# Performance work log

Measured on AMD Instinct MI355X. Metric: run time of the kernel, lower is better.

The kernel has to match this reference:

```python
import jax, jax.numpy as jnp
import numpy as np

N_MID, EMB_DIM, HID, SEQ_LEN, BATCH = 200000, 128, 128, 256, 512


def setup_inputs() -> dict:
    key = jax.random.key(0)
    k1, k2, k3, k4, k5, k6, k7 = jax.random.split(key, 7)
    mid = jax.random.randint(k1, (BATCH,), 0, N_MID, dtype=jnp.int32)
    mid_hist = jax.random.randint(k2, (BATCH, SEQ_LEN), 0, N_MID, dtype=jnp.int32)
    mask = jax.random.randint(k3, (BATCH, SEQ_LEN), 0, 2, dtype=jnp.int32)
    # Embedding table: RandomUniform(-0.05, 0.05) per original init
    emb_table = jax.random.uniform(k4, (N_MID, EMB_DIM), jnp.float32, -0.05, 0.05)
    # Keras GRU (reset_after=True): kernel [D,3H], recurrent_kernel [H,3H], bias [2,3H]
    W = jax.random.normal(k5, (EMB_DIM, 3 * HID), jnp.float32) * 0.05
    U = jax.random.normal(k6, (HID, 3 * HID), jnp.float32) * 0.05
    b = jax.random.normal(k7, (2, 3 * HID), jnp.float32) * 0.05
    return {"mid": mid, "mid_hist": mid_hist, "mask": mask,
            "emb_table": emb_table, "W": W, "U": U, "b": b}


def _masked_gru(hist_emb, mask, W, U, b):
    # hist_emb: [B, T, D], mask: [B, T] int
    B, T, _ = hist_emb.shape
    H = U.shape[0]
    b_in, b_rec = b[0], b[1]
    # precompute input projections once: [B, T, 3H]
    x_proj = jnp.einsum('btd,dh->bth', hist_emb, W) + b_in
    x_proj_t = jnp.swapaxes(x_proj, 0, 1)  # [T, B, 3H]
    mask_t = jnp.swapaxes(mask, 0, 1).astype(bool)  # [T, B]

    def step(h, inp):
        x_t, m_t = inp
        rec = h @ U + b_rec  # [B, 3H]
        xz, xr, xh = x_t[:, :H], x_t[:, H:2 * H], x_t[:, 2 * H:]
        rz, rr, rh = rec[:, :H], rec[:, H:2 * H], rec[:, 2 * H:]
        z = jax.nn.sigmoid(xz + rz)
        r = jax.nn.sigmoid(xr + rr)
        hh = jnp.tanh(xh + r * rh)  # reset_after=True: r applied after recurrent matmul
        h_new = z * h + (1.0 - z) * hh
        h = jnp.where(m_t[:, None], h_new, h)  # masked steps hold state
        return h, None

    h0 = jnp.zeros((B, H), hist_emb.dtype)
    h_final, _ = jax.lax.scan(step, h0, (x_proj_t, mask_t))
    return h_final


def reference(mid, mid_hist, mask, emb_table, W, U, b):
    item_emb = emb_table[mid]            # [B, D]
    hist_emb = emb_table[mid_hist]       # [B, T, D]
    user_vec = _masked_gru(hist_emb, mask, W, U, b)  # [B, H]
    return (user_vec, item_emb)
```

## Files before the change

### kernel.cpp

```cpp
#include <hip/hip_runtime.h>

#define BATCH  512
#define SEQLEN 256
#define EMB    128
#define HID    128

typedef _Float16 f16;
typedef __attribute__((ext_vector_type(8))) _Float16 half8;
typedef __attribute__((ext_vector_type(4))) _Float16 half4f;
typedef __attribute__((ext_vector_type(4))) float    floatx4;

#define L2E 1.44269504088896340736f
#define T2E 2.88539008177792681472f

__device__ __forceinline__ int swzB(int byte) {
    return byte ^ (((byte >> 8) & 7) << 4);
}

__global__ void prep_kernel(const int* __restrict__ mask, const int* __restrict__ mid,
                            const float* __restrict__ emb,
                            unsigned* __restrict__ maskP, float* __restrict__ item_out) {
    const int bid = blockIdx.x, tid = threadIdx.x;
    if (bid < 32) {
        __shared__ int mls[16 * 256];
        for (int i = tid; i < 16 * 256; i += 256)
            mls[i] = mask[bid * 16 * 256 + i];
        __syncthreads();
        int t = tid;
        unsigned m = 0;
        #pragma unroll
        for (int r = 0; r < 16; ++r)
            m |= (unsigned)(mls[r * 256 + t] & 1) << r;
        maskP[bid * 256 + t] = m;
    } else {
        for (int i = (bid - 32) * 256 + tid; i < BATCH * EMB; i += 224 * 256) {
            int b = i >> 7, d = i & 127;
            item_out[i] = emb[(size_t)mid[b] * EMB + d];
        }
    }
}

__global__ __launch_bounds__(512, 2) void gru_fused(
        const int* __restrict__ mid_hist, const float* __restrict__ emb,
        const float* __restrict__ W, const float* __restrict__ U,
        const float* __restrict__ bvec, const unsigned* __restrict__ maskP,
        float* __restrict__ out_user) {
    __shared__ __align__(16) f16 hpk[2][16 * 128];
    __shared__ __align__(16) f16 elds[4][16 * 128];

    const int tid   = threadIdx.x;
    const int lane  = tid & 63;
    const int w     = tid >> 6;
    const int l15   = lane & 15;
    const int g4    = lane >> 4;
    const int blk   = blockIdx.x;
    const int bbase = blk * 16;

    half8 uA[3][4], wA[3][4];
    #pragma unroll
    for (int p = 0; p < 3; ++p)
        #pragma unroll
        for (int kt = 0; kt < 4; ++kt) {
            half8 u, v;
            const int j = p * 128 + w * 16 + l15;
            #pragma unroll
            for (int e = 0; e < 8; ++e) {
                int k = kt * 32 + g4 * 8 + e;
                u[e] = (f16)U[k * 384 + j];
                v[e] = (f16)W[k * 384 + j];
            }
            uA[p][kt] = u; wA[p][kt] = v;
        }

    const int jj = w * 16 + g4 * 4;
    float nbz[4], nbr[4], sxh[4], srh[4];
    {
        float4 a0 = *(const float4*)(bvec + jj);
        float4 a1 = *(const float4*)(bvec + 384 + jj);
        float4 c0 = *(const float4*)(bvec + 128 + jj);
        float4 c1 = *(const float4*)(bvec + 512 + jj);
        float4 d0 = *(const float4*)(bvec + 256 + jj);
        float4 d1 = *(const float4*)(bvec + 640 + jj);
        nbz[0] = -L2E*(a0.x+a1.x); nbz[1] = -L2E*(a0.y+a1.y);
        nbz[2] = -L2E*(a0.z+a1.z); nbz[3] = -L2E*(a0.w+a1.w);
        nbr[0] = -L2E*(c0.x+c1.x); nbr[1] = -L2E*(c0.y+c1.y);
        nbr[2] = -L2E*(c0.z+c1.z); nbr[3] = -L2E*(c0.w+c1.w);
        sxh[0] =  T2E*d0.x; sxh[1] = T2E*d0.y; sxh[2] = T2E*d0.z; sxh[3] = T2E*d0.w;
        srh[0] =  T2E*d1.x; srh[1] = T2E*d1.y; srh[2] = T2E*d1.z; srh[3] = T2E*d1.w;
    }

    int aswz[4];
    #pragma unroll
    for (int kt = 0; kt < 4; ++kt)
        aswz[kt] = swzB(l15 * 256 + kt * 64 + g4 * 16) >> 1;
    const int hswz = swzB(l15 * 256 + jj * 2) >> 1;
    const int r_e  = tid >> 5;
    const int c32  = tid & 31;
    const int sswz = swzB(r_e * 256 + c32 * 8) >> 1;
    const int histbase = (bbase + r_e) * SEQLEN;
    const int mpbase   = blk * SEQLEN;

    for (int i = tid; i < 16 * 128; i += 512) hpk[0][i] = (f16)0.f;

    {
        int i0 = mid_hist[histbase + 0];
        int i1 = mid_hist[histbase + 1];
        float4 v0 = *(const float4*)(emb + (size_t)i0 * EMB + c32 * 4);
        float4 v1 = *(const float4*)(emb + (size_t)i1 * EMB + c32 * 4);
        *(half4f*)&elds[0][sswz] = half4f{(f16)v0.x,(f16)v0.y,(f16)v0.z,(f16)v0.w};
        *(half4f*)&elds[1][sswz] = half4f{(f16)v1.x,(f16)v1.y,(f16)v1.z,(f16)v1.w};
    }
    int i2 = mid_hist[histbase + 2];
    int i3 = mid_hist[histbase + 3];
    float4   Ee = *(const float4*)(emb + (size_t)i2 * EMB + c32 * 4);
    float4   Eo = *(const float4*)(emb + (size_t)i3 * EMB + c32 * 4);
    int      Ie = mid_hist[histbase + 4];
    int      Io = mid_hist[histbase + 5];
    unsigned Me = maskP[mpbase + 0];
    unsigned Mo = maskP[mpbase + 1];

    float hreg[4] = {0.f, 0.f, 0.f, 0.f};
    __syncthreads();

    half8 ea[4];
    #pragma unroll
    for (int kt = 0; kt < 4; ++kt) ea[kt] = *(const half8*)&elds[0][aswz[kt]];

    auto step = [&](int t, float4& E, int& I, unsigned& M) {
        const f16* hrd = hpk[t & 1];
        f16*       hwr = hpk[(t + 1) & 1];
        half8 ha[4];
        #pragma unroll
        for (int kt = 0; kt < 4; ++kt) ha[kt] = *(const half8*)&hrd[aswz[kt]];

        floatx4 az = {0,0,0,0}, ar = {0,0,0,0}, axh = {0,0,0,0}, arh = {0,0,0,0};
        #pragma unroll
        for (int kt = 0; kt < 4; ++kt) {
            az  = __builtin_amdgcn_mfma_f32_16x16x32_f16(wA[0][kt], ea[kt], az,  0,0,0);
            ar  = __builtin_amdgcn_mfma_f32_16x16x32_f16(wA[1][kt], ea[kt], ar,  0,0,0);
            axh = __builtin_amdgcn_mfma_f32_16x16x32_f16(wA[2][kt], ea[kt], axh, 0,0,0);
        }
        #pragma unroll
        for (int kt = 0; kt < 4; ++kt) {
            az  = __builtin_amdgcn_mfma_f32_16x16x32_f16(uA[0][kt], ha[kt], az,  0,0,0);
            ar  = __builtin_amdgcn_mfma_f32_16x16x32_f16(uA[1][kt], ha[kt], ar,  0,0,0);
            arh = __builtin_amdgcn_mfma_f32_16x16x32_f16(uA[2][kt], ha[kt], arh, 0,0,0);
        }

        *(half4f*)&elds[(t + 2) & 3][sswz] =
            half4f{(f16)E.x, (f16)E.y, (f16)E.z, (f16)E.w};
        int ii = I;
        E = *(const float4*)(emb + (size_t)ii * EMB + c32 * 4);
        int t6 = t + 6 < SEQLEN ? t + 6 : SEQLEN - 1;
        I = mid_hist[histbase + t6];
        unsigned mval = M;
        M = maskP[mpbase + t + 2];
        {
            const f16* erd = elds[(t + 1) & 3];
            #pragma unroll
            for (int kt = 0; kt < 4; ++kt) ea[kt] = *(const half8*)&erd[aswz[kt]];
        }

        const int mbit = (mval >> l15) & 1;
        #pragma unroll
        for (int r = 0; r < 4; ++r) {
            float z  = __builtin_amdgcn_rcpf(1.f + __builtin_amdgcn_exp2f(__builtin_fmaf(az[r], -L2E, nbz[r])));
            float rg = __builtin_amdgcn_rcpf(1.f + __builtin_amdgcn_exp2f(__builtin_fmaf(ar[r], -L2E, nbr[r])));
            float u  = __builtin_fmaf(rg, __builtin_fmaf(arh[r], T2E, srh[r]),
                                          __builtin_fmaf(axh[r], T2E, sxh[r]));
            float hh = __builtin_fmaf(-2.f, __builtin_amdgcn_rcpf(__builtin_amdgcn_exp2f(u) + 1.f), 1.f);
            float hn = __builtin_fmaf(z, hreg[r] - hh, hh);
            hreg[r]  = mbit ? hn : hreg[r];
        }
        *(half4f*)&hwr[hswz] = half4f{(f16)hreg[0], (f16)hreg[1], (f16)hreg[2], (f16)hreg[3]};

        __builtin_amdgcn_sched_barrier(0);
        asm volatile("s_waitcnt lgkmcnt(0)" ::: "memory");
        __builtin_amdgcn_s_barrier();
        __builtin_amdgcn_sched_barrier(0);
    };

    #pragma unroll 1
    for (int t = 0; t < SEQLEN; t += 2) {
        step(t,     Ee, Ie, Me);
        step(t + 1, Eo, Io, Mo);
    }

    float4 o = { hreg[0], hreg[1], hreg[2], hreg[3] };
    *(float4*)(out_user + (size_t)(bbase + l15) * HID + jj) = o;
}

extern "C" void kernel_launch(void* const* d_in, const int* in_sizes, int n_in,
                              void* d_out, int out_size, void* d_ws, size_t ws_size,
                              hipStream_t stream) {
    const int*   mid      = (const int*)d_in[0];
    const int*   mid_hist = (const int*)d_in[1];
    const int*   mask     = (const int*)d_in[2];
    const float* emb      = (const float*)d_in[3];
    const float* W        = (const float*)d_in[4];
    const float* U        = (const float*)d_in[5];
    const float* bvec     = (const float*)d_in[6];

    float* user_out = (float*)d_out;
    float* item_out = (float*)d_out + BATCH * HID;

    unsigned* maskP = (unsigned*)d_ws;

    prep_kernel<<<256, 256, 0, stream>>>(mask, mid, emb, maskP, item_out);
    gru_fused  <<<32, 512, 0, stream>>>(mid_hist, emb, W, U, bvec, maskP, user_out);
}
```

Before: 353.1 us.

## Precompute next step's input projection MFMAs off the recurrent critical path

Moves the W·x input-projection MFMAs for step t+1 into step t, after the recurrent U·h MFMAs, so each step's dependent chain starts directly from h. The log2e/2log2e activation scales are folded into the fp16 W and U weights, which removes per-element scaling FMAs in the gate math. The cost is more live accumulator registers (two XAcc sets) and slightly different fp16 rounding of the weights. The mask prefetch index is also clamped to avoid reading past the end.

Result: no change. 355.8 us (+0.8%).

```diff
diff --git a/kernel.cpp b/kernel.cpp
--- a/kernel.cpp
+++ b/kernel.cpp
@@ -16,6 +16,8 @@
 __device__ __forceinline__ int swzB(int byte) {
     return byte ^ (((byte >> 8) & 7) << 4);
 }
+
+struct XAcc { floatx4 z, r, h; };
 
 __global__ void prep_kernel(const int* __restrict__ mask, const int* __restrict__ mid,
                             const float* __restrict__ emb,
@@ -58,7 +60,8 @@
 
     half8 uA[3][4], wA[3][4];
     #pragma unroll
-    for (int p = 0; p < 3; ++p)
+    for (int p = 0; p < 3; ++p) {
+        const float s = (p == 2) ? T2E : -L2E;
         #pragma unroll
         for (int kt = 0; kt < 4; ++kt) {
             half8 u, v;
@@ -66,11 +69,12 @@
             #pragma unroll
             for (int e = 0; e < 8; ++e) {
                 int k = kt * 32 + g4 * 8 + e;
-                u[e] = (f16)U[k * 384 + j];
-                v[e] = (f16)W[k * 384 + j];
+                u[e] = (f16)(U[k * 384 + j] * s);
+                v[e] = (f16)(W[k * 384 + j] * s);
             }
             uA[p][kt] = u; wA[p][kt] = v;
         }
+    }
 
     const int jj = w * 16 + g4 * 4;
     float nbz[4], nbr[4], sxh[4], srh[4];
@@ -122,29 +126,47 @@
     float hreg[4] = {0.f, 0.f, 0.f, 0.f};
     __syncthreads();
 
-    half8 ea[4];
-    #pragma unroll
-    for (int kt = 0; kt < 4; ++kt) ea[kt] = *(const half8*)&elds[0][aswz[kt]];
-
-    auto step = [&](int t, float4& E, int& I, unsigned& M) {
+    XAcc xA, xB;
+    {
+        half8 e0[4];
+        #pragma unroll
+        for (int kt = 0; kt < 4; ++kt) e0[kt] = *(const half8*)&elds[0][aswz[kt]];
+        xA.z = floatx4{0,0,0,0}; xA.r = floatx4{0,0,0,0}; xA.h = floatx4{0,0,0,0};
+        #pragma unroll
+        for (int kt = 0; kt < 4; ++kt) {
+            xA.z = __builtin_amdgcn_mfma_f32_16x16x32_f16(wA[0][kt], e0[kt], xA.z, 0,0,0);
+            xA.r = __builtin_amdgcn_mfma_f32_16x16x32_f16(wA[1][kt], e0[kt], xA.r, 0,0,0);
+            xA.h = __builtin_amdgcn_mfma_f32_16x16x32_f16(wA[2][kt], e0[kt], xA.h, 0,0,0);
+        }
+    }
+
+    auto step = [&](int t, XAcc& xc, XAcc& xn, float4& E, int& I, unsigned& M) {
         const f16* hrd = hpk[t & 1];
         f16*       hwr = hpk[(t + 1) & 1];
+
         half8 ha[4];
         #pragma unroll
         for (int kt = 0; kt < 4; ++kt) ha[kt] = *(const half8*)&hrd[aswz[kt]];
-
-        floatx4 az = {0,0,0,0}, ar = {0,0,0,0}, axh = {0,0,0,0}, arh = {0,0,0,0};
+        floatx4 arh = {0,0,0,0};
         #pragma unroll
         for (int kt = 0; kt < 4; ++kt) {
-            az  = __builtin_amdgcn_mfma_f32_16x16x32_f16(wA[0][kt], ea[kt], az,  0,0,0);
-            ar  = __builtin_amdgcn_mfma_f32_16x16x32_f16(wA[1][kt], ea[kt], ar,  0,0,0);
-            axh = __builtin_amdgcn_mfma_f32_16x16x32_f16(wA[2][kt], ea[kt], axh, 0,0,0);
-        }
-        #pragma unroll
-        for (int kt = 0; kt < 4; ++kt) {
-            az  = __builtin_amdgcn_mfma_f32_16x16x32_f16(uA[0][kt], ha[kt], az,  0,0,0);
-            ar  = __builtin_amdgcn_mfma_f32_16x16x32_f16(uA[1][kt], ha[kt], ar,  0,0,0);
-            arh = __builtin_amdgcn_mfma_f32_16x16x32_f16(uA[2][kt], ha[kt], arh, 0,0,0);
+            xc.z = __builtin_amdgcn_mfma_f32_16x16x32_f16(uA[0][kt], ha[kt], xc.z, 0,0,0);
+            xc.r = __builtin_amdgcn_mfma_f32_16x16x32_f16(uA[1][kt], ha[kt], xc.r, 0,0,0);
+            arh  = __builtin_amdgcn_mfma_f32_16x16x32_f16(uA[2][kt], ha[kt], arh,  0,0,0);
+        }
+
+        {
+            const f16* erd = elds[(t + 1) & 3];
+            half8 ea[4];
+            #pragma unroll
+            for (int kt = 0; kt < 4; ++kt) ea[kt] = *(const half8*)&erd[aswz[kt]];
+            xn.z = floatx4{0,0,0,0}; xn.r = floatx4{0,0,0,0}; xn.h = floatx4{0,0,0,0};
+            #pragma unroll
+            for (int kt = 0; kt < 4; ++kt) {
+                xn.z = __builtin_amdgcn_mfma_f32_16x16x32_f16(wA[0][kt], ea[kt], xn.z, 0,0,0);
+                xn.r = __builtin_amdgcn_mfma_f32_16x16x32_f16(wA[1][kt], ea[kt], xn.r, 0,0,0);
+                xn.h = __builtin_amdgcn_mfma_f32_16x16x32_f16(wA[2][kt], ea[kt], xn.h, 0,0,0);
+            }
         }
 
         *(half4f*)&elds[(t + 2) & 3][sswz] =
@@ -154,20 +176,15 @@
         int t6 = t + 6 < SEQLEN ? t + 6 : SEQLEN - 1;
         I = mid_hist[histbase + t6];
         unsigned mval = M;
-        M = maskP[mpbase + t + 2];
-        {
-            const f16* erd = elds[(t + 1) & 3];
-            #pragma unroll
-            for (int kt = 0; kt < 4; ++kt) ea[kt] = *(const half8*)&erd[aswz[kt]];
-        }
+        int tm = t + 2 < SEQLEN ? t + 2 : SEQLEN - 1;
+        M = maskP[mpbase + tm];
 
         const int mbit = (mval >> l15) & 1;
         #pragma unroll
         for (int r = 0; r < 4; ++r) {
-            float z  = __builtin_amdgcn_rcpf(1.f + __builtin_amdgcn_exp2f(__builtin_fmaf(az[r], -L2E, nbz[r])));
-            float rg = __builtin_amdgcn_rcpf(1.f + __builtin_amdgcn_exp2f(__builtin_fmaf(ar[r], -L2E, nbr[r])));
-            float u  = __builtin_fmaf(rg, __builtin_fmaf(arh[r], T2E, srh[r]),
-                                          __builtin_fmaf(axh[r], T2E, sxh[r]));
+            float z  = __builtin_amdgcn_rcpf(1.f + __builtin_amdgcn_exp2f(xc.z[r] + nbz[r]));
+            float rg = __builtin_amdgcn_rcpf(1.f + __builtin_amdgcn_exp2f(xc.r[r] + nbr[r]));
+            float u  = __builtin_fmaf(rg, arh[r] + srh[r], xc.h[r] + sxh[r]);
             float hh = __builtin_fmaf(-2.f, __builtin_amdgcn_rcpf(__builtin_amdgcn_exp2f(u) + 1.f), 1.f);
             float hn = __builtin_fmaf(z, hreg[r] - hh, hh);
             hreg[r]  = mbit ? hn : hreg[r];
@@ -182,8 +199,8 @@
 
     #pragma unroll 1
     for (int t = 0; t < SEQLEN; t += 2) {
-        step(t,     Ee, Ie, Me);
-        step(t + 1, Eo, Io, Mo);
+        step(t,     xA, xB, Ee, Ie, Me);
+        step(t + 1, xB, xA, Eo, Io, Mo);
     }
 
     float4 o = { hreg[0], hreg[1], hreg[2], hreg[3] };
```
